# Optimization experiments

Hardware: AMD Instinct MI355X
Metric: run time of the kernel (lower is better)

Reference implementation:

```python
import jax, jax.numpy as jnp
import numpy as np


def setup_inputs() -> dict:
    key = jax.random.key(0)
    k1, k2 = jax.random.split(key)
    B1, B2, S0, K = 16, 16, 64, 64  # K = state_size
    e1 = jax.random.normal(k1, (B1, B2, 2, S0, K), dtype=jnp.float32)
    e2 = jax.random.normal(k2, (B1, B2, 2, K, K), dtype=jnp.float32)
    return {"e1": e1, "e2": e2}


def reference(e1, e2):
    # Faithful to CheckNodeTrellis.call (batch_dims=2):
    # res[b1,b2,u1,s0,s2] = logsumexp_{u2 in {0,1}, s1 in [K]}(
    #     e1[b1,b2,(u1+u2)%2,s0,s1] + e2[b1,b2,u2,s1,s2] )
    # The original builds meshgrid/tile gather_nd indices; here the index
    # arithmetic is expressed algebraically via a 2x2 parity table + broadcast.
    parity = (jnp.arange(2)[:, None] + jnp.arange(2)[None, :]) % 2  # [u1, u2]
    E1 = e1[:, :, parity, :, :]                    # [B1,B2,u1,u2,S0,K]
    # terms: [B1,B2,u1,u2,S0,s1,s2]
    terms = E1[..., None] + e2[:, :, None, :, None, :, :]
    # reduce over u2 (axis 3) and s1 (axis 5)
    return jax.scipy.special.logsumexp(terms, axis=(3, 5))
```

## Files before the change

kernel.cpp:

```cpp
#include <hip/hip_runtime.h>


typedef short short4v __attribute__((ext_vector_type(4)));
typedef short short8v __attribute__((ext_vector_type(8)));
typedef float float4v __attribute__((ext_vector_type(4)));

#define LDA 72
#define LDB 68

__device__ __forceinline__ short expbf(float x) {
    float f = __expf(x);
    unsigned u = __builtin_bit_cast(unsigned, f);
    u += 0x7fffu + ((u >> 16) & 1u);
    return (short)(u >> 16);
}

__global__ __launch_bounds__(256) void trellis_mfma_kernel(
    const float* __restrict__ e1,
    const float* __restrict__ e2,
    float* __restrict__ out)
{
    __shared__ __align__(16) short A0s[32 * LDA];
    __shared__ __align__(16) short A1s[32 * LDA];
    __shared__ __align__(16) short B0s[64 * LDB];
    __shared__ __align__(16) short B1s[64 * LDB];

    const int tid  = threadIdx.x;
    const int pair = blockIdx.x & 255;
    const int h    = blockIdx.x >> 8;
    const size_t base = (size_t)pair * 8192;

    const float4* __restrict__ e1v = (const float4*)(e1 + base);
    const float4* __restrict__ e2v = (const float4*)(e2 + base);

    #pragma unroll
    for (int it = 0; it < 2; ++it) {
        const int f = it * 256 + tid;
        const int r = f >> 4, c4 = f & 15;
        const float4 a0 = e1v[h * 512 + f];
        const float4 a1 = e1v[1024 + h * 512 + f];
        short4v p0, p1;
        p0.x = expbf(a0.x); p0.y = expbf(a0.y); p0.z = expbf(a0.z); p0.w = expbf(a0.w);
        p1.x = expbf(a1.x); p1.y = expbf(a1.y); p1.z = expbf(a1.z); p1.w = expbf(a1.w);
        *(short4v*)&A0s[r * LDA + c4 * 4] = p0;
        *(short4v*)&A1s[r * LDA + c4 * 4] = p1;
    }
    #pragma unroll
    for (int it = 0; it < 4; ++it) {
        const int f = it * 256 + tid;
        const int k = f >> 4, c4 = f & 15;
        const float4 b0 = e2v[f];
        const float4 b1 = e2v[1024 + f];
        short4v p0, p1;
        p0.x = expbf(b0.x); p0.y = expbf(b0.y); p0.z = expbf(b0.z); p0.w = expbf(b0.w);
        p1.x = expbf(b1.x); p1.y = expbf(b1.y); p1.z = expbf(b1.z); p1.w = expbf(b1.w);
        *(short4v*)&B0s[k * LDB + c4 * 4] = p0;
        *(short4v*)&B1s[k * LDB + c4 * 4] = p1;
    }
    __syncthreads();

    const int w    = tid >> 6;
    const int lane = tid & 63;
    const int ln   = lane & 15;
    const int g    = lane >> 4;
    const int r0   = (w >> 1) * 16;
    const int c0   = (w & 1) * 32;

    short8v a0f[2], a1f[2];
    #pragma unroll
    for (int ks = 0; ks < 2; ++ks) {
        const int off = (r0 + ln) * LDA + ks * 32 + g * 8;
        a0f[ks] = *(const short8v*)&A0s[off];
        a1f[ks] = *(const short8v*)&A1s[off];
    }

    short8v b0f[2][2], b1f[2][2];
    #pragma unroll
    for (int ct = 0; ct < 2; ++ct) {
        #pragma unroll
        for (int ks = 0; ks < 2; ++ks) {
            const int col = c0 + ct * 16 + ln;
            const int kb  = ks * 32 + g * 8;
            short8v t0, t1;
            #pragma unroll
            for (int i = 0; i < 8; ++i) {
                t0[i] = B0s[(kb + i) * LDB + col];
                t1[i] = B1s[(kb + i) * LDB + col];
            }
            b0f[ct][ks] = t0;
            b1f[ct][ks] = t1;
        }
    }

    float4v acc0[2] = {{0.f,0.f,0.f,0.f}, {0.f,0.f,0.f,0.f}};
    float4v acc1[2] = {{0.f,0.f,0.f,0.f}, {0.f,0.f,0.f,0.f}};
    #pragma unroll
    for (int ct = 0; ct < 2; ++ct) {
        #pragma unroll
        for (int ks = 0; ks < 2; ++ks) {
            acc0[ct] = __builtin_amdgcn_mfma_f32_16x16x32_bf16(a0f[ks], b0f[ct][ks], acc0[ct], 0, 0, 0);
            acc0[ct] = __builtin_amdgcn_mfma_f32_16x16x32_bf16(a1f[ks], b1f[ct][ks], acc0[ct], 0, 0, 0);
            acc1[ct] = __builtin_amdgcn_mfma_f32_16x16x32_bf16(a1f[ks], b0f[ct][ks], acc1[ct], 0, 0, 0);
            acc1[ct] = __builtin_amdgcn_mfma_f32_16x16x32_bf16(a0f[ks], b1f[ct][ks], acc1[ct], 0, 0, 0);
        }
    }

    const int srow0 = 32 * h + r0 + g * 4;
    #pragma unroll
    for (int ct = 0; ct < 2; ++ct) {
        const int col = c0 + ct * 16 + ln;
        #pragma unroll
        for (int j = 0; j < 4; ++j) {
            const size_t o = base + (size_t)(srow0 + j) * 64 + col;
            out[o]        = __logf(acc0[ct][j]);
            out[o + 4096] = __logf(acc1[ct][j]);
        }
    }
}

extern "C" void kernel_launch(void* const* d_in, const int* in_sizes, int n_in,
                              void* d_out, int out_size, void* d_ws, size_t ws_size,
                              hipStream_t stream)
{
    const float* e1 = (const float*)d_in[0];
    const float* e2 = (const float*)d_in[1];
    float* out = (float*)d_out;
    hipLaunchKernelGGL(trellis_mfma_kernel, dim3(512), dim3(256), 0, stream,
                       e1, e2, out);
}
```

Before: 69.39 us.

## Process whole batch pair per 512-thread block to avoid duplicate e2 loads

Merges the two half-row blocks per (b1,b2) pair into one 512-thread block covering all 64 rows. The e2 matrices are loaded and exponentiated once per pair instead of twice. Warps are remapped so each handles one column tile and two row tiles. This halves the grid to 256 blocks, which may reduce latency hiding.

```diff
diff --git a/kernel.cpp b/kernel.cpp
--- a/kernel.cpp
+++ b/kernel.cpp
@@ -15,30 +15,28 @@
     return (short)(u >> 16);
 }
 
-__global__ __launch_bounds__(256) void trellis_mfma_kernel(
+__global__ __launch_bounds__(512) void trellis_mfma_kernel(
     const float* __restrict__ e1,
     const float* __restrict__ e2,
     float* __restrict__ out)
 {
-    __shared__ __align__(16) short A0s[32 * LDA];
-    __shared__ __align__(16) short A1s[32 * LDA];
+    __shared__ __align__(16) short A0s[64 * LDA];
+    __shared__ __align__(16) short A1s[64 * LDA];
     __shared__ __align__(16) short B0s[64 * LDB];
     __shared__ __align__(16) short B1s[64 * LDB];
 
-    const int tid  = threadIdx.x;
-    const int pair = blockIdx.x & 255;
-    const int h    = blockIdx.x >> 8;
-    const size_t base = (size_t)pair * 8192;
+    const int tid = threadIdx.x;
+    const size_t base = (size_t)blockIdx.x * 8192;
 
     const float4* __restrict__ e1v = (const float4*)(e1 + base);
     const float4* __restrict__ e2v = (const float4*)(e2 + base);
 
     #pragma unroll
     for (int it = 0; it < 2; ++it) {
-        const int f = it * 256 + tid;
+        const int f = it * 512 + tid;
         const int r = f >> 4, c4 = f & 15;
-        const float4 a0 = e1v[h * 512 + f];
-        const float4 a1 = e1v[1024 + h * 512 + f];
+        const float4 a0 = e1v[f];
+        const float4 a1 = e1v[1024 + f];
         short4v p0, p1;
         p0.x = expbf(a0.x); p0.y = expbf(a0.y); p0.z = expbf(a0.z); p0.w = expbf(a0.w);
         p1.x = expbf(a1.x); p1.y = expbf(a1.y); p1.z = expbf(a1.z); p1.w = expbf(a1.w);
@@ -46,8 +44,8 @@
         *(short4v*)&A1s[r * LDA + c4 * 4] = p1;
     }
     #pragma unroll
-    for (int it = 0; it < 4; ++it) {
-        const int f = it * 256 + tid;
+    for (int it = 0; it < 2; ++it) {
+        const int f = it * 512 + tid;
         const int k = f >> 4, c4 = f & 15;
         const float4 b0 = e2v[f];
         const float4 b1 = e2v[1024 + f];
@@ -63,57 +61,57 @@
     const int lane = tid & 63;
     const int ln   = lane & 15;
     const int g    = lane >> 4;
-    const int r0   = (w >> 1) * 16;
-    const int c0   = (w & 1) * 32;
+    const int ct   = w & 3;
+    const int rb   = (w >> 2) * 16;
 
-    short8v a0f[2], a1f[2];
+    short8v a0f[2][2], a1f[2][2];
+    #pragma unroll
+    for (int t = 0; t < 2; ++t) {
+        #pragma unroll
+        for (int ks = 0; ks < 2; ++ks) {
+            const int off = (rb + t * 32 + ln) * LDA + ks * 32 + g * 8;
+            a0f[t][ks] = *(const short8v*)&A0s[off];
+            a1f[t][ks] = *(const short8v*)&A1s[off];
+        }
+    }
+
+    short8v b0f[2], b1f[2];
     #pragma unroll
     for (int ks = 0; ks < 2; ++ks) {
-        const int off = (r0 + ln) * LDA + ks * 32 + g * 8;
-        a0f[ks] = *(const short8v*)&A0s[off];
-        a1f[ks] = *(const short8v*)&A1s[off];
-    }
-
-    short8v b0f[2][2], b1f[2][2];
-    #pragma unroll
-    for (int ct = 0; ct < 2; ++ct) {
+        const int kb  = ks * 32 + g * 8;
+        const int col = ct * 16 + ln;
+        short8v t0, t1;
         #pragma unroll
-        for (int ks = 0; ks < 2; ++ks) {
-            const int col = c0 + ct * 16 + ln;
-            const int kb  = ks * 32 + g * 8;
-            short8v t0, t1;
-            #pragma unroll
-            for (int i = 0; i < 8; ++i) {
-                t0[i] = B0s[(kb + i) * LDB + col];
-                t1[i] = B1s[(kb + i) * LDB + col];
-            }
-            b0f[ct][ks] = t0;
-            b1f[ct][ks] = t1;
+        for (int i = 0; i < 8; ++i) {
+            t0[i] = B0s[(kb + i) * LDB + col];
+            t1[i] = B1s[(kb + i) * LDB + col];
         }
+        b0f[ks] = t0;
+        b1f[ks] = t1;
     }
 
     float4v acc0[2] = {{0.f,0.f,0.f,0.f}, {0.f,0.f,0.f,0.f}};
     float4v acc1[2] = {{0.f,0.f,0.f,0.f}, {0.f,0.f,0.f,0.f}};
     #pragma unroll
-    for (int ct = 0; ct < 2; ++ct) {
+    for (int t = 0; t < 2; ++t) {
         #pragma unroll
         for (int ks = 0; ks < 2; ++ks) {
-            acc0[ct] = __builtin_amdgcn_mfma_f32_16x16x32_bf16(a0f[ks], b0f[ct][ks], acc0[ct], 0, 0, 0);
-            acc0[ct] = __builtin_amdgcn_mfma_f32_16x16x32_bf16(a1f[ks], b1f[ct][ks], acc0[ct], 0, 0, 0);
-            acc1[ct] = __builtin_amdgcn_mfma_f32_16x16x32_bf16(a1f[ks], b0f[ct][ks], acc1[ct], 0, 0, 0);
-            acc1[ct] = __builtin_amdgcn_mfma_f32_16x16x32_bf16(a0f[ks], b1f[ct][ks], acc1[ct], 0, 0, 0);
+            acc0[t] = __builtin_amdgcn_mfma_f32_16x16x32_bf16(a0f[t][ks], b0f[ks], acc0[t], 0, 0, 0);
+            acc0[t] = __builtin_amdgcn_mfma_f32_16x16x32_bf16(a1f[t][ks], b1f[ks], acc0[t], 0, 0, 0);
+            acc1[t] = __builtin_amdgcn_mfma_f32_16x16x32_bf16(a1f[t][ks], b0f[ks], acc1[t], 0, 0, 0);
+            acc1[t] = __builtin_amdgcn_mfma_f32_16x16x32_bf16(a0f[t][ks], b1f[ks], acc1[t], 0, 0, 0);
         }
     }
 
-    const int srow0 = 32 * h + r0 + g * 4;
     #pragma unroll
-    for (int ct = 0; ct < 2; ++ct) {
-        const int col = c0 + ct * 16 + ln;
+    for (int t = 0; t < 2; ++t) {
+        const int srow0 = rb + t * 32 + g * 4;
+        const int col   = ct * 16 + ln;
         #pragma unroll
         for (int j = 0; j < 4; ++j) {
             const size_t o = base + (size_t)(srow0 + j) * 64 + col;
-            out[o]        = __logf(acc0[ct][j]);
-            out[o + 4096] = __logf(acc1[ct][j]);
+            out[o]        = __logf(acc0[t][j]);
+            out[o + 4096] = __logf(acc1[t][j]);
         }
     }
 }
@@ -125,6 +123,6 @@
     const float* e1 = (const float*)d_in[0];
     const float* e2 = (const float*)d_in[1];
     float* out = (float*)d_out;
-    hipLaunchKernelGGL(trellis_mfma_kernel, dim3(512), dim3(256), 0, stream,
+    hipLaunchKernelGGL(trellis_mfma_kernel, dim3(256), dim3(512), 0, stream,
                        e1, e2, out);
 }
```

After: 69.40 us. About the same (+0.0%).
